# Kernel optimization log

Hardware: AMD Instinct MI355X
Metric: run time of the kernel (lower is better)

## Reference

```python
import jax, jax.numpy as jnp
import numpy as np

DIM = 768
NUM_HEADS = 12
HEAD_DIM = DIM // NUM_HEADS
EPS = 1e-5


def setup_inputs() -> dict:
    key = jax.random.key(0)
    ks = jax.random.split(key, 12)
    s = 0.02
    return {
        "x": jax.random.normal(ks[0], (8, 1024, DIM), jnp.float32),
        "pos_embed": jax.random.normal(ks[1], (8, 1024, DIM), jnp.float32),
        "gamma": jnp.ones((DIM,), jnp.float32),
        "beta": jnp.zeros((DIM,), jnp.float32),
        "Wq": jax.random.normal(ks[2], (DIM, DIM), jnp.float32) * s,
        "bq": jnp.zeros((DIM,), jnp.float32),
        "Wk": jax.random.normal(ks[3], (DIM, DIM), jnp.float32) * s,
        "bk": jnp.zeros((DIM,), jnp.float32),
        "Wv": jax.random.normal(ks[4], (DIM, DIM), jnp.float32) * s,
        "bv": jnp.zeros((DIM,), jnp.float32),
        "Wo": jax.random.normal(ks[5], (DIM, DIM), jnp.float32) * s,
        "bo": jnp.zeros((DIM,), jnp.float32),
    }


def _split_heads(t):
    B, N, C = t.shape
    return t.reshape(B, N, NUM_HEADS, HEAD_DIM).transpose(0, 2, 1, 3)  # (B,H,N,D)


def reference(x, pos_embed, gamma, beta, Wq, bq, Wk, bk, Wv, bv, Wo, bo):
    B, N, C = x.shape
    # pre-LayerNorm
    mu = jnp.mean(x, axis=-1, keepdims=True)
    var = jnp.mean(jnp.square(x - mu), axis=-1, keepdims=True)
    x_norm = (x - mu) * jax.lax.rsqrt(var + EPS) * gamma + beta

    Q = _split_heads(x_norm @ Wq + bq) + _split_heads(pos_embed)  # pos-embed added to Q
    K = _split_heads(x_norm @ Wk + bk)
    V = _split_heads(x_norm @ Wv + bv)

    inv_temp = 1.0 / jnp.sqrt(jnp.float32(HEAD_DIM))
    S = jnp.einsum("bhnd,bhmd->bhnm", Q, K) * inv_temp  # (B,H,N,N)
    A = jax.nn.softmax(S, axis=-1)  # dropout p=0.0 -> identity
    vals = jnp.einsum("bhnm,bhmd->bhnd", A, V)
    vals = vals.transpose(0, 2, 1, 3).reshape(B, N, C)
    return vals @ Wo + bo + x  # residual
```

## Files before the change

kernel.cpp:

```cpp
#include <hip/hip_runtime.h>
#include <hip/hip_bf16.h>

#define TOK 8192
#define CDIM 768
#define NH 12
#define HD 64
#define QKV_N 2304
#define QSCALE 0.18033688011f
#define MREF 10.0f

typedef __attribute__((ext_vector_type(8))) short bf16x8;
typedef __attribute__((ext_vector_type(4))) float f32x4;
typedef unsigned short ushort_t;

__device__ __forceinline__ ushort_t f2bf(float f) {
  unsigned u = __float_as_uint(f);
  u += 0x7fffu + ((u >> 16) & 1u);
  return (ushort_t)(u >> 16);
}

__device__ __forceinline__ f32x4 mfma16(bf16x8 a, bf16x8 b, f32x4 c) {
  return __builtin_amdgcn_mfma_f32_16x16x32_bf16(a, b, c, 0, 0, 0);
}

__device__ __forceinline__ int swz(int r) { return (r ^ (r >> 3)) & 7; }

__device__ __forceinline__ void gload16(const void* g, void* l) {
  __builtin_amdgcn_global_load_lds(
      (const __attribute__((address_space(1))) unsigned int*)g,
      (__attribute__((address_space(3))) unsigned int*)l, 16, 0, 0);
}

__global__ __launch_bounds__(256) void ln_kernel(const float* __restrict__ x,
                                                 const float* __restrict__ gamma,
                                                 const float* __restrict__ beta,
                                                 ushort_t* __restrict__ xn) {
  int t = blockIdx.x;
  const float* row = x + (size_t)t * CDIM;
  float v[3];
  float s = 0.f, s2 = 0.f;
#pragma unroll
  for (int i = 0; i < 3; i++) {
    v[i] = row[threadIdx.x + 256 * i];
    s += v[i];
    s2 += v[i] * v[i];
  }
#pragma unroll
  for (int off = 32; off; off >>= 1) {
    s += __shfl_xor(s, off);
    s2 += __shfl_xor(s2, off);
  }
  __shared__ float red[8];
  int wid = threadIdx.x >> 6, lane = threadIdx.x & 63;
  if (lane == 0) { red[wid] = s; red[wid + 4] = s2; }
  __syncthreads();
  s = red[0] + red[1] + red[2] + red[3];
  s2 = red[4] + red[5] + red[6] + red[7];
  float mu = s * (1.f / CDIM);
  float var = s2 * (1.f / CDIM) - mu * mu;
  float rstd = rsqrtf(var + 1e-5f);
  ushort_t* orow = xn + (size_t)t * CDIM;
#pragma unroll
  for (int i = 0; i < 3; i++) {
    int c = threadIdx.x + 256 * i;
    orow[c] = f2bf((v[i] - mu) * rstd * gamma[c] + beta[c]);
  }
}

__global__ __launch_bounds__(256) void wtrans_kernel(const float* __restrict__ Wq,
                                                     const float* __restrict__ Wk,
                                                     const float* __restrict__ Wv,
                                                     const float* __restrict__ Wo,
                                                     ushort_t* __restrict__ wt) {
  const float* W = (blockIdx.z == 0) ? Wq : (blockIdx.z == 1) ? Wk
                   : (blockIdx.z == 2) ? Wv : Wo;
  __shared__ float tile[32][33];
  int tr = blockIdx.y, tc = blockIdx.x;
  int tx = threadIdx.x, ty = threadIdx.y;
#pragma unroll
  for (int j = 0; j < 4; j++) {
    int k = tr * 32 + ty + j * 8;
    tile[ty + j * 8][tx] = W[(size_t)k * CDIM + tc * 32 + tx];
  }
  __syncthreads();
  ushort_t* o = wt + (size_t)blockIdx.z * CDIM * CDIM;
#pragma unroll
  for (int j = 0; j < 4; j++) {
    int n = tc * 32 + ty + j * 8;
    o[(size_t)n * CDIM + tr * 32 + tx] = f2bf(tile[tx][ty + j * 8]);
  }
}

template <int MODE>
__global__ __launch_bounds__(256) void gemm_kernel(
    const ushort_t* __restrict__ A, const ushort_t* __restrict__ Bt,
    const float* __restrict__ b0, const float* __restrict__ b1,
    const float* __restrict__ b2, const float* __restrict__ extra,
    void* __restrict__ outp) {
  __shared__ __align__(16) ushort_t lds_a[2][128 * 64];
  __shared__ __align__(16) ushort_t lds_b[2][128 * 64];
  const int NB = (MODE == 0) ? 18 : 6;
  int lin = blockIdx.y * NB + blockIdx.x;
  int nl = (lin & 7) * (NB * 8) + (lin >> 3);
  const int bn = nl % NB, bm = nl / NB;

  const int tid = threadIdx.x;
  const int lane = tid & 63, wid = tid >> 6;
  const int wr = wid >> 1, wc = wid & 1;
  const int l16 = lane & 15, lg = lane >> 4;
  f32x4 acc[4][4] = {};

  int aoff[2][4], boff[2][4];
#pragma unroll
  for (int kk = 0; kk < 2; kk++) {
#pragma unroll
    for (int mi = 0; mi < 4; mi++) {
      int r = wr * 64 + mi * 16 + l16;
      aoff[kk][mi] = r * 64 + (((kk * 4 + lg) ^ swz(r)) & 7) * 8;
    }
#pragma unroll
    for (int ni = 0; ni < 4; ni++) {
      int r = wc * 64 + ni * 16 + l16;
      boff[kk][ni] = r * 64 + (((kk * 4 + lg) ^ swz(r)) & 7) * 8;
    }
  }

  auto stage = [&](int buf, int k0) {
#pragma unroll
    for (int i = 0; i < 4; i++) {
      int slot = i * 256 + tid;
      int row = slot >> 3, j = slot & 7;
      int c8 = ((j ^ swz(row)) & 7) * 8;
      gload16(&A[(size_t)(bm * 128 + row) * CDIM + k0 + c8], &lds_a[buf][slot * 8]);
      gload16(&Bt[(size_t)(bn * 128 + row) * CDIM + k0 + c8], &lds_b[buf][slot * 8]);
    }
  };

  stage(0, 0);
  asm volatile("s_waitcnt vmcnt(0)" ::: "memory");
  __builtin_amdgcn_s_barrier();
  __builtin_amdgcn_sched_barrier(0);

  int cur = 0;
#pragma unroll 2
  for (int t = 0; t < 12; t++) {
    if (t < 11) stage(cur ^ 1, (t + 1) * 64);
#pragma unroll
    for (int kk = 0; kk < 2; kk++) {
      bf16x8 af[4], bfr[4];
#pragma unroll
      for (int mi = 0; mi < 4; mi++)
        af[mi] = *reinterpret_cast<const bf16x8*>(&lds_a[cur][aoff[kk][mi]]);
#pragma unroll
      for (int ni = 0; ni < 4; ni++)
        bfr[ni] = *reinterpret_cast<const bf16x8*>(&lds_b[cur][boff[kk][ni]]);
      __builtin_amdgcn_s_setprio(1);
#pragma unroll
      for (int mi = 0; mi < 4; mi++)
#pragma unroll
        for (int ni = 0; ni < 4; ni++)
          acc[mi][ni] = mfma16(af[mi], bfr[ni], acc[mi][ni]);
      __builtin_amdgcn_s_setprio(0);
    }
    asm volatile("s_waitcnt vmcnt(0) lgkmcnt(0)" ::: "memory");
    __builtin_amdgcn_s_barrier();
    __builtin_amdgcn_sched_barrier(0);
    cur ^= 1;
  }

#pragma unroll
  for (int mi = 0; mi < 4; mi++)
#pragma unroll
    for (int ni = 0; ni < 4; ni++)
#pragma unroll
      for (int r = 0; r < 4; r++) {
        int grow = bm * 128 + wr * 64 + mi * 16 + 4 * lg + r;
        int gcol = bn * 128 + wc * 64 + ni * 16 + l16;
        float v = acc[mi][ni][r];
        if (MODE == 0) {
          if (gcol < 768) {
            v = (v + b0[gcol] + extra[(size_t)grow * CDIM + gcol]) * QSCALE;
          } else if (gcol < 1536) {
            v += b1[gcol - 768];
          } else {
            v += b2[gcol - 1536];
          }
          ((ushort_t*)outp)[(size_t)grow * QKV_N + gcol] = f2bf(v);
        } else {
          v += b0[gcol] + extra[(size_t)grow * CDIM + gcol];
          ((float*)outp)[(size_t)grow * CDIM + gcol] = v;
        }
      }
}

__global__ __launch_bounds__(256, 3) void attn_kernel(const ushort_t* __restrict__ QKV,
                                                      ushort_t* __restrict__ O) {
  const int b = blockIdx.x, h = blockIdx.y, qt = blockIdx.z;

  const int tid = threadIdx.x, lane = tid & 63, w = tid >> 6;
  const int l16 = lane & 15, lg = lane >> 4;
  const int tb = b * 1024 + qt * 128;
  const int co_q = h * HD, co_k = CDIM + h * HD, co_v = 2 * CDIM + h * HD;

  __shared__ __align__(16) ushort_t k_lds[2][64 * 64];
  __shared__ __align__(16) ushort_t vt_lds[2][64 * 64];
  __shared__ __align__(16) ushort_t p_lds[128 * 64];

  bf16x8 qf[2][2];
#pragma unroll
  for (int mi = 0; mi < 2; mi++)
#pragma unroll
    for (int ds = 0; ds < 2; ds++)
      qf[mi][ds] = *reinterpret_cast<const bf16x8*>(
          &QKV[(size_t)(tb + w * 32 + mi * 16 + l16) * QKV_N + co_q + ds * 32 + 8 * lg]);

  float m_sm[2] = {MREF, MREF};
  float l_sm[2] = {0.f, 0.f};
  float m_acc[2][4];
#pragma unroll
  for (int mi = 0; mi < 2; mi++)
#pragma unroll
    for (int r = 0; r < 4; r++) m_acc[mi][r] = MREF;
  f32x4 oacc[2][4] = {};

  int kfoff[2][4];
#pragma unroll
  for (int ds = 0; ds < 2; ds++)
#pragma unroll
    for (int ni = 0; ni < 4; ni++) {
      int rr = ni * 16 + l16;
      kfoff[ds][ni] = rr * 64 + (((ds * 4 + lg) ^ swz(rr)) & 7) * 8;
    }
  int poff[2][4], paoff[2][2];
#pragma unroll
  for (int mi = 0; mi < 2; mi++) {
    int myq = w * 32 + mi * 16 + l16;
    int sq = swz(myq);
#pragma unroll
    for (int ni = 0; ni < 4; ni++)
      poff[mi][ni] = myq * 64 + (lg & 1) * 4 + (((ni * 2 + (lg >> 1)) ^ sq) & 7) * 8;
#pragma unroll
    for (int ks = 0; ks < 2; ks++)
      paoff[mi][ks] = myq * 64 + (((ks * 4 + lg) ^ sq) & 7) * 8;
  }
  int vboff[2][4];
#pragma unroll
  for (int ks = 0; ks < 2; ks++)
#pragma unroll
    for (int ni = 0; ni < 4; ni++) {
      int d = ni * 16 + l16;
      vboff[ks][ni] = d * 64 + (((ks * 4 + lg) ^ swz(d)) & 7) * 8;
    }

  auto stage_k = [&](int buf, int kt) {
    const int kv0 = kt * 64;
#pragma unroll
    for (int i = 0; i < 2; i++) {
      int slot = i * 256 + tid;
      int r = slot >> 3, j = slot & 7;
      int c = ((j ^ swz(r)) & 7) * 8;
      gload16(&QKV[(size_t)(b * 1024 + kv0 + r) * QKV_N + co_k + c],
              &k_lds[buf][slot * 8]);
    }
  };

  const int kv0 = (tid >> 3) * 2, d0 = (tid & 7) * 8;
  const int sV = ((kv0 >> 3) ^ (d0 >> 3)) & 7;
  int voff[8];
#pragma unroll
  for (int u = 0; u < 8; u++)
    voff[u] = (d0 + u) * 64 + ((sV ^ u) & 7) * 8 + (kv0 & 7);
  const ushort_t* vsrc = QKV + (size_t)(b * 1024 + kv0) * QKV_N + co_v + d0;

  uint4 vr0, vr1;
  auto load_v = [&](int kt) {
    vr0 = *reinterpret_cast<const uint4*>(vsrc + (size_t)kt * 64 * QKV_N);
    vr1 = *reinterpret_cast<const uint4*>(vsrc + (size_t)kt * 64 * QKV_N + QKV_N);
  };
  auto write_v = [&](int buf) {
    const unsigned* w0 = reinterpret_cast<const unsigned*>(&vr0);
    const unsigned* w1 = reinterpret_cast<const unsigned*>(&vr1);
#pragma unroll
    for (int u = 0; u < 8; u++) {
      unsigned a = w0[u >> 1], c = w1[u >> 1];
      unsigned val = (u & 1) ? ((a >> 16) | (c & 0xffff0000u))
                             : ((a & 0xffffu) | (c << 16));
      *reinterpret_cast<unsigned*>(&vt_lds[buf][voff[u]]) = val;
    }
  };

  stage_k(0, 0);
  load_v(0);
  write_v(0);
  asm volatile("s_waitcnt vmcnt(0) lgkmcnt(0)" ::: "memory");
  __builtin_amdgcn_s_barrier();
  __builtin_amdgcn_sched_barrier(0);

  for (int kt = 0; kt < 16; kt++) {
    const int cur = kt & 1, nxt = cur ^ 1;
    if (kt < 15) { stage_k(nxt, kt + 1); load_v(kt + 1); }

    bf16x8 kf[2][4];
#pragma unroll
    for (int ds = 0; ds < 2; ds++)
#pragma unroll
      for (int ni = 0; ni < 4; ni++)
        kf[ds][ni] = *reinterpret_cast<const bf16x8*>(&k_lds[cur][kfoff[ds][ni]]);

#pragma unroll
    for (int mi = 0; mi < 2; mi++) {
      f32x4 st[4] = {};
      __builtin_amdgcn_s_setprio(1);
#pragma unroll
      for (int ds = 0; ds < 2; ds++)
#pragma unroll
        for (int ni = 0; ni < 4; ni++)
          st[ni] = mfma16(kf[ds][ni], qf[mi][ds], st[ni]);
      __builtin_amdgcn_s_setprio(0);

      float t0 = fmaxf(fmaxf(st[0][0], st[0][1]), fmaxf(st[0][2], st[0][3]));
      float t1 = fmaxf(fmaxf(st[1][0], st[1][1]), fmaxf(st[1][2], st[1][3]));
      float t2 = fmaxf(fmaxf(st[2][0], st[2][1]), fmaxf(st[2][2], st[2][3]));
      float t3 = fmaxf(fmaxf(st[3][0], st[3][1]), fmaxf(st[3][2], st[3][3]));
      float tm = fmaxf(fmaxf(t0, t1), fmaxf(t2, t3));

      if (__any(tm > m_sm[mi])) {
        float rm = fmaxf(tm, __shfl_xor(tm, 16));
        rm = fmaxf(rm, __shfl_xor(rm, 32));
        float mnew = fmaxf(m_sm[mi], rm);
        l_sm[mi] *= exp2f(m_sm[mi] - mnew);
        m_sm[mi] = mnew;
#pragma unroll
        for (int r = 0; r < 4; r++) {
          float mn = __shfl(mnew, 4 * lg + r);
          float corr = exp2f(m_acc[mi][r] - mn);
          m_acc[mi][r] = mn;
#pragma unroll
          for (int ni = 0; ni < 4; ni++) oacc[mi][ni][r] *= corr;
        }
      }

      float ps[4];
#pragma unroll
      for (int ni = 0; ni < 4; ni++) {
        float e0 = exp2f(st[ni][0] - m_sm[mi]);
        float e1 = exp2f(st[ni][1] - m_sm[mi]);
        float e2 = exp2f(st[ni][2] - m_sm[mi]);
        float e3 = exp2f(st[ni][3] - m_sm[mi]);
        st[ni][0] = e0; st[ni][1] = e1; st[ni][2] = e2; st[ni][3] = e3;
        ps[ni] = (e0 + e1) + (e2 + e3);
      }
      l_sm[mi] += (ps[0] + ps[1]) + (ps[2] + ps[3]);

#pragma unroll
      for (int ni = 0; ni < 4; ni++) {
        unsigned p01, p23;
        asm("v_cvt_pk_bf16_f32 %0, %1, %2" : "=v"(p01) : "v"(st[ni][0]), "v"(st[ni][1]));
        asm("v_cvt_pk_bf16_f32 %0, %1, %2" : "=v"(p23) : "v"(st[ni][2]), "v"(st[ni][3]));
        uint2 pk; pk.x = p01; pk.y = p23;
        *reinterpret_cast<uint2*>(&p_lds[poff[mi][ni]]) = pk;
      }
    }

#pragma unroll
    for (int ks = 0; ks < 2; ks++) {
      bf16x8 pa0 = *reinterpret_cast<const bf16x8*>(&p_lds[paoff[0][ks]]);
      bf16x8 pa1 = *reinterpret_cast<const bf16x8*>(&p_lds[paoff[1][ks]]);
      bf16x8 vb[4];
#pragma unroll
      for (int ni = 0; ni < 4; ni++)
        vb[ni] = *reinterpret_cast<const bf16x8*>(&vt_lds[cur][vboff[ks][ni]]);
      __builtin_amdgcn_s_setprio(1);
#pragma unroll
      for (int ni = 0; ni < 4; ni++) {
        oacc[0][ni] = mfma16(pa0, vb[ni], oacc[0][ni]);
        oacc[1][ni] = mfma16(pa1, vb[ni], oacc[1][ni]);
      }
      __builtin_amdgcn_s_setprio(0);
    }

    if (kt < 15) write_v(nxt);
    asm volatile("s_waitcnt vmcnt(0) lgkmcnt(0)" ::: "memory");
    __builtin_amdgcn_s_barrier();
    __builtin_amdgcn_sched_barrier(0);
  }

#pragma unroll
  for (int mi = 0; mi < 2; mi++) {
    float l = l_sm[mi];
    l += __shfl_xor(l, 16);
    l += __shfl_xor(l, 32);
#pragma unroll
    for (int r = 0; r < 4; r++) {
      float lr = __shfl(l, 4 * lg + r);
      float inv = 1.f / lr;
      int grow = tb + w * 32 + mi * 16 + 4 * lg + r;
#pragma unroll
      for (int ni = 0; ni < 4; ni++) {
        int gcol = h * HD + ni * 16 + l16;
        O[(size_t)grow * CDIM + gcol] = f2bf(oacc[mi][ni][r] * inv);
      }
    }
  }
}

extern "C" void kernel_launch(void* const* d_in, const int* in_sizes, int n_in,
                              void* d_out, int out_size, void* d_ws, size_t ws_size,
                              hipStream_t stream) {
  const float* x     = (const float*)d_in[0];
  const float* pos   = (const float*)d_in[1];
  const float* gamma = (const float*)d_in[2];
  const float* beta  = (const float*)d_in[3];
  const float* Wq    = (const float*)d_in[4];
  const float* bq    = (const float*)d_in[5];
  const float* Wk    = (const float*)d_in[6];
  const float* bk    = (const float*)d_in[7];
  const float* Wv    = (const float*)d_in[8];
  const float* bv    = (const float*)d_in[9];
  const float* Wo    = (const float*)d_in[10];
  const float* bo    = (const float*)d_in[11];
  float* out = (float*)d_out;

  ushort_t* xn   = (ushort_t*)d_ws;
  ushort_t* wt   = xn + (size_t)TOK * CDIM;
  ushort_t* qkv  = wt + (size_t)3072 * CDIM;
  ushort_t* aout = qkv + (size_t)TOK * QKV_N;

  ln_kernel<<<TOK, 256, 0, stream>>>(x, gamma, beta, xn);
  wtrans_kernel<<<dim3(24, 24, 4), dim3(32, 8), 0, stream>>>(Wq, Wk, Wv, Wo, wt);
  gemm_kernel<0><<<dim3(18, 64), 256, 0, stream>>>(xn, wt, bq, bk, bv, pos, qkv);
  attn_kernel<<<dim3(8, NH, 8), 256, 0, stream>>>(qkv, aout);
  gemm_kernel<1><<<dim3(6, 64), 256, 0, stream>>>(aout, wt + (size_t)QKV_N * CDIM,
                                                  bo, nullptr, nullptr, x, out);
}
```

Before: 167.5 us.

## Use 256x256 tiles with 512 threads for the QKV projection GEMM

```diff
diff --git a/kernel.cpp b/kernel.cpp
--- a/kernel.cpp
+++ b/kernel.cpp
@@ -91,15 +91,119 @@
   }
 }
 
-template <int MODE>
-__global__ __launch_bounds__(256) void gemm_kernel(
+__global__ __launch_bounds__(512) void gemm0_kernel(
     const ushort_t* __restrict__ A, const ushort_t* __restrict__ Bt,
-    const float* __restrict__ b0, const float* __restrict__ b1,
-    const float* __restrict__ b2, const float* __restrict__ extra,
-    void* __restrict__ outp) {
+    const float* __restrict__ bq, const float* __restrict__ bk,
+    const float* __restrict__ bv, const float* __restrict__ pos,
+    ushort_t* __restrict__ outp) {
+  __shared__ __align__(16) ushort_t lds_a[2][256 * 64];
+  __shared__ __align__(16) ushort_t lds_b[2][256 * 64];
+  int lin = blockIdx.y * 9 + blockIdx.x;
+  int nl = (lin & 7) * 36 + (lin >> 3);
+  const int bn = nl % 9, bm = nl / 9;
+
+  const int tid = threadIdx.x;
+  const int lane = tid & 63, wid = tid >> 6;
+  const int wr = wid >> 2, wc = wid & 3;
+  const int l16 = lane & 15, lg = lane >> 4;
+  f32x4 acc[8][4] = {};
+
+  int aoff[2][8], boff[2][4];
+#pragma unroll
+  for (int kk = 0; kk < 2; kk++) {
+#pragma unroll
+    for (int mi = 0; mi < 8; mi++) {
+      int r = wr * 128 + mi * 16 + l16;
+      aoff[kk][mi] = r * 64 + (((kk * 4 + lg) ^ swz(r)) & 7) * 8;
+    }
+#pragma unroll
+    for (int ni = 0; ni < 4; ni++) {
+      int r = wc * 64 + ni * 16 + l16;
+      boff[kk][ni] = r * 64 + (((kk * 4 + lg) ^ swz(r)) & 7) * 8;
+    }
+  }
+
+  auto stageA = [&](int buf, int k0, int u) {
+    int s = u * 512 + tid;
+    int row = s >> 3, j = s & 7;
+    int c8 = ((j ^ swz(row)) & 7) * 8;
+    gload16(&A[(size_t)(bm * 256 + row) * CDIM + k0 + c8], &lds_a[buf][s * 8]);
+  };
+  auto stageB = [&](int buf, int k0, int u) {
+    int s = u * 512 + tid;
+    int row = s >> 3, j = s & 7;
+    int c8 = ((j ^ swz(row)) & 7) * 8;
+    gload16(&Bt[(size_t)(bn * 256 + row) * CDIM + k0 + c8], &lds_b[buf][s * 8]);
+  };
+
+#pragma unroll
+  for (int u = 0; u < 4; u++) { stageA(0, 0, u); stageB(0, 0, u); }
+  asm volatile("s_waitcnt vmcnt(0)" ::: "memory");
+  __builtin_amdgcn_s_barrier();
+
+  int cur = 0;
+  for (int t = 0; t < 12; t++) {
+    const int k0n = (t + 1) * 64;
+    const bool st = (t < 11);
+    bf16x8 bf[2][4];
+#pragma unroll
+    for (int kk = 0; kk < 2; kk++)
+#pragma unroll
+      for (int ni = 0; ni < 4; ni++)
+        bf[kk][ni] = *reinterpret_cast<const bf16x8*>(&lds_b[cur][boff[kk][ni]]);
+
+#pragma unroll
+    for (int p = 0; p < 4; p++) {
+      if (st) { stageA(cur ^ 1, k0n, p); stageB(cur ^ 1, k0n, p); }
+      bf16x8 af[2][2];
+#pragma unroll
+      for (int kk = 0; kk < 2; kk++)
+#pragma unroll
+        for (int q = 0; q < 2; q++)
+          af[kk][q] = *reinterpret_cast<const bf16x8*>(
+              &lds_a[cur][aoff[kk][2 * p + q]]);
+      __builtin_amdgcn_s_setprio(1);
+#pragma unroll
+      for (int kk = 0; kk < 2; kk++)
+#pragma unroll
+        for (int q = 0; q < 2; q++)
+#pragma unroll
+          for (int ni = 0; ni < 4; ni++)
+            acc[2 * p + q][ni] = mfma16(af[kk][q], bf[kk][ni], acc[2 * p + q][ni]);
+      __builtin_amdgcn_s_setprio(0);
+    }
+    asm volatile("s_waitcnt vmcnt(0) lgkmcnt(0)" ::: "memory");
+    __builtin_amdgcn_s_barrier();
+    cur ^= 1;
+  }
+
+#pragma unroll
+  for (int mi = 0; mi < 8; mi++)
+#pragma unroll
+    for (int ni = 0; ni < 4; ni++)
+#pragma unroll
+      for (int r = 0; r < 4; r++) {
+        int grow = bm * 256 + wr * 128 + mi * 16 + 4 * lg + r;
+        int gcol = bn * 256 + wc * 64 + ni * 16 + l16;
+        float v = acc[mi][ni][r];
+        if (gcol < 768) {
+          v = (v + bq[gcol] + pos[(size_t)grow * CDIM + gcol]) * QSCALE;
+        } else if (gcol < 1536) {
+          v += bk[gcol - 768];
+        } else {
+          v += bv[gcol - 1536];
+        }
+        outp[(size_t)grow * QKV_N + gcol] = f2bf(v);
+      }
+}
+
+__global__ __launch_bounds__(256) void gemm1_kernel(
+    const ushort_t* __restrict__ A, const ushort_t* __restrict__ Bt,
+    const float* __restrict__ b0, const float* __restrict__ extra,
+    float* __restrict__ outp) {
   __shared__ __align__(16) ushort_t lds_a[2][128 * 64];
   __shared__ __align__(16) ushort_t lds_b[2][128 * 64];
-  const int NB = (MODE == 0) ? 18 : 6;
+  const int NB = 6;
   int lin = blockIdx.y * NB + blockIdx.x;
   int nl = (lin & 7) * (NB * 8) + (lin >> 3);
   const int bn = nl % NB, bm = nl / NB;
@@ -176,20 +280,8 @@
       for (int r = 0; r < 4; r++) {
         int grow = bm * 128 + wr * 64 + mi * 16 + 4 * lg + r;
         int gcol = bn * 128 + wc * 64 + ni * 16 + l16;
-        float v = acc[mi][ni][r];
-        if (MODE == 0) {
-          if (gcol < 768) {
-            v = (v + b0[gcol] + extra[(size_t)grow * CDIM + gcol]) * QSCALE;
-          } else if (gcol < 1536) {
-            v += b1[gcol - 768];
-          } else {
-            v += b2[gcol - 1536];
-          }
-          ((ushort_t*)outp)[(size_t)grow * QKV_N + gcol] = f2bf(v);
-        } else {
-          v += b0[gcol] + extra[(size_t)grow * CDIM + gcol];
-          ((float*)outp)[(size_t)grow * CDIM + gcol] = v;
-        }
+        outp[(size_t)grow * CDIM + gcol] =
+            acc[mi][ni][r] + b0[gcol] + extra[(size_t)grow * CDIM + gcol];
       }
 }
 
@@ -428,8 +520,8 @@
 
   ln_kernel<<<TOK, 256, 0, stream>>>(x, gamma, beta, xn);
   wtrans_kernel<<<dim3(24, 24, 4), dim3(32, 8), 0, stream>>>(Wq, Wk, Wv, Wo, wt);
-  gemm_kernel<0><<<dim3(18, 64), 256, 0, stream>>>(xn, wt, bq, bk, bv, pos, qkv);
+  gemm0_kernel<<<dim3(9, 32), 512, 0, stream>>>(xn, wt, bq, bk, bv, pos, qkv);
   attn_kernel<<<dim3(8, NH, 8), 256, 0, stream>>>(qkv, aout);
-  gemm_kernel<1><<<dim3(6, 64), 256, 0, stream>>>(aout, wt + (size_t)QKV_N * CDIM,
-                                                  bo, nullptr, nullptr, x, out);
-}
+  gemm1_kernel<<<dim3(6, 64), 256, 0, stream>>>(aout, wt + (size_t)QKV_N * CDIM,
+                                                bo, x, out);
+}
```

Result: slower. 186.6 us (+11.4%).

## Replace QKV projection GEMM with simple single-buffered padded-LDS kernel

Applied to the files above, without the earlier changes.

```diff
diff --git a/kernel.cpp b/kernel.cpp
--- a/kernel.cpp
+++ b/kernel.cpp
@@ -91,15 +91,73 @@
   }
 }
 
-template <int MODE>
-__global__ __launch_bounds__(256) void gemm_kernel(
+__global__ __launch_bounds__(256) void gemm0_kernel(
     const ushort_t* __restrict__ A, const ushort_t* __restrict__ Bt,
-    const float* __restrict__ b0, const float* __restrict__ b1,
-    const float* __restrict__ b2, const float* __restrict__ extra,
-    void* __restrict__ outp) {
+    const float* __restrict__ bq, const float* __restrict__ bk,
+    const float* __restrict__ bv, const float* __restrict__ pos,
+    ushort_t* __restrict__ outp) {
+  __shared__ __align__(16) ushort_t lds_a[128][40];
+  __shared__ __align__(16) ushort_t lds_b[128][40];
+  const int bn = blockIdx.x, bm = blockIdx.y;
+  const int tid = threadIdx.x;
+  const int lane = tid & 63, wid = tid >> 6;
+  const int wr = wid >> 1, wc = wid & 1;
+  const int l16 = lane & 15, lg = lane >> 4;
+  f32x4 acc[4][4] = {};
+
+  for (int k0 = 0; k0 < CDIM; k0 += 32) {
+#pragma unroll
+    for (int i = 0; i < 2; i++) {
+      int ch = tid + 256 * i;
+      int row = ch >> 2, c8 = (ch & 3) * 8;
+      *reinterpret_cast<uint4*>(&lds_a[row][c8]) =
+          *reinterpret_cast<const uint4*>(&A[(size_t)(bm * 128 + row) * CDIM + k0 + c8]);
+      *reinterpret_cast<uint4*>(&lds_b[row][c8]) =
+          *reinterpret_cast<const uint4*>(&Bt[(size_t)(bn * 128 + row) * CDIM + k0 + c8]);
+    }
+    __syncthreads();
+    bf16x8 af[4], bfr[4];
+#pragma unroll
+    for (int mi = 0; mi < 4; mi++)
+      af[mi] = *reinterpret_cast<const bf16x8*>(&lds_a[wr * 64 + mi * 16 + l16][8 * lg]);
+#pragma unroll
+    for (int ni = 0; ni < 4; ni++)
+      bfr[ni] = *reinterpret_cast<const bf16x8*>(&lds_b[wc * 64 + ni * 16 + l16][8 * lg]);
+#pragma unroll
+    for (int mi = 0; mi < 4; mi++)
+#pragma unroll
+      for (int ni = 0; ni < 4; ni++)
+        acc[mi][ni] = mfma16(af[mi], bfr[ni], acc[mi][ni]);
+    __syncthreads();
+  }
+
+#pragma unroll
+  for (int mi = 0; mi < 4; mi++)
+#pragma unroll
+    for (int ni = 0; ni < 4; ni++)
+#pragma unroll
+      for (int r = 0; r < 4; r++) {
+        int grow = bm * 128 + wr * 64 + mi * 16 + 4 * lg + r;
+        int gcol = bn * 128 + wc * 64 + ni * 16 + l16;
+        float v = acc[mi][ni][r];
+        if (gcol < 768) {
+          v = (v + bq[gcol] + pos[(size_t)grow * CDIM + gcol]) * QSCALE;
+        } else if (gcol < 1536) {
+          v += bk[gcol - 768];
+        } else {
+          v += bv[gcol - 1536];
+        }
+        outp[(size_t)grow * QKV_N + gcol] = f2bf(v);
+      }
+}
+
+__global__ __launch_bounds__(256) void gemm1_kernel(
+    const ushort_t* __restrict__ A, const ushort_t* __restrict__ Bt,
+    const float* __restrict__ b0, const float* __restrict__ extra,
+    float* __restrict__ outp) {
   __shared__ __align__(16) ushort_t lds_a[2][128 * 64];
   __shared__ __align__(16) ushort_t lds_b[2][128 * 64];
-  const int NB = (MODE == 0) ? 18 : 6;
+  const int NB = 6;
   int lin = blockIdx.y * NB + blockIdx.x;
   int nl = (lin & 7) * (NB * 8) + (lin >> 3);
   const int bn = nl % NB, bm = nl / NB;
@@ -176,20 +234,8 @@
       for (int r = 0; r < 4; r++) {
         int grow = bm * 128 + wr * 64 + mi * 16 + 4 * lg + r;
         int gcol = bn * 128 + wc * 64 + ni * 16 + l16;
-        float v = acc[mi][ni][r];
-        if (MODE == 0) {
-          if (gcol < 768) {
-            v = (v + b0[gcol] + extra[(size_t)grow * CDIM + gcol]) * QSCALE;
-          } else if (gcol < 1536) {
-            v += b1[gcol - 768];
-          } else {
-            v += b2[gcol - 1536];
-          }
-          ((ushort_t*)outp)[(size_t)grow * QKV_N + gcol] = f2bf(v);
-        } else {
-          v += b0[gcol] + extra[(size_t)grow * CDIM + gcol];
-          ((float*)outp)[(size_t)grow * CDIM + gcol] = v;
-        }
+        outp[(size_t)grow * CDIM + gcol] =
+            acc[mi][ni][r] + b0[gcol] + extra[(size_t)grow * CDIM + gcol];
       }
 }
 
@@ -428,8 +474,8 @@
 
   ln_kernel<<<TOK, 256, 0, stream>>>(x, gamma, beta, xn);
   wtrans_kernel<<<dim3(24, 24, 4), dim3(32, 8), 0, stream>>>(Wq, Wk, Wv, Wo, wt);
-  gemm_kernel<0><<<dim3(18, 64), 256, 0, stream>>>(xn, wt, bq, bk, bv, pos, qkv);
+  gemm0_kernel<<<dim3(18, 64), 256, 0, stream>>>(xn, wt, bq, bk, bv, pos, qkv);
   attn_kernel<<<dim3(8, NH, 8), 256, 0, stream>>>(qkv, aout);
-  gemm_kernel<1><<<dim3(6, 64), 256, 0, stream>>>(aout, wt + (size_t)QKV_N * CDIM,
-                                                  bo, nullptr, nullptr, x, out);
-}
+  gemm1_kernel<<<dim3(6, 64), 256, 0, stream>>>(aout, wt + (size_t)QKV_N * CDIM,
+                                                bo, x, out);
+}
```

After: 172.6 us. 3.1% more time.
